# Kernel tuning notes

Hardware: AMD Instinct MI355X
Metric: run time of the kernel (lower is better)

The kernel has to match this reference:

```python
import jax, jax.numpy as jnp
import numpy as np

N = 100000       # nodes
E = 1600000      # edges (avg degree 16)
IN_DIM = 128
HIDDEN = 128


def _glorot(key, shape):
    s = 1.0 / np.sqrt(shape[0])
    return jax.random.uniform(key, shape, minval=-s, maxval=s, dtype=jnp.float32)


def setup_inputs() -> dict:
    key = jax.random.key(0)
    ks = jax.random.split(key, 8)
    x = jax.random.normal(ks[0], (N, IN_DIM), dtype=jnp.float32)
    edge_index = jax.random.randint(ks[1], (2, E), 0, N, dtype=jnp.int32)
    W0 = _glorot(ks[2], (IN_DIM, HIDDEN))
    b0 = jnp.zeros((HIDDEN,), dtype=jnp.float32)
    W1 = _glorot(ks[3], (HIDDEN, HIDDEN))
    b1 = jnp.zeros((HIDDEN,), dtype=jnp.float32)
    W2 = _glorot(ks[4], (HIDDEN, HIDDEN))
    b2 = jnp.zeros((HIDDEN,), dtype=jnp.float32)
    return {"x": x, "edge_index": edge_index,
            "W0": W0, "b0": b0, "W1": W1, "b1": b1, "W2": W2, "b2": b2}


def _gcn_conv(x, row, col, norm, W, b):
    # x' = W x, then out[i] = sum_{j in N(i) U {i}} norm_ji * x'[j], + bias
    h = x @ W                              # [N, out]
    msg = norm[:, None] * h[row]           # [E+N, out] gather + scale
    out = jax.ops.segment_sum(msg, col, num_segments=N)  # scatter-add
    return out + b


def reference(x, edge_index, W0, b0, W1, b1, W2, b2):
    # PyG GCNConv default: add self-loops, symmetric normalization D^-1/2 A D^-1/2
    self_loops = jnp.arange(N, dtype=edge_index.dtype)
    row = jnp.concatenate([edge_index[0], self_loops])  # sources
    col = jnp.concatenate([edge_index[1], self_loops])  # destinations
    deg = jax.ops.segment_sum(jnp.ones_like(col, dtype=x.dtype), col, num_segments=N)
    dinv = jax.lax.rsqrt(deg)              # deg >= 1 thanks to self-loops
    norm = dinv[row] * dinv[col]           # [E+N]

    h = _gcn_conv(x, row, col, norm, W0, b0)
    h = jax.nn.relu(h)                     # dropout: eval mode (identity)
    h = _gcn_conv(h, row, col, norm, W1, b1)
    h = jax.nn.relu(h)
    return _gcn_conv(h, row, col, norm, W2, b2)
```

## Files before the change

### kernel.cpp

```cpp
#include <hip/hip_runtime.h>

#define HID 128
#define BR  128
#define FILL_CHUNK 2048

typedef _Float16 f16;
typedef f16 f16x2 __attribute__((ext_vector_type(2)));
typedef f16 f16x4 __attribute__((ext_vector_type(4)));
typedef f16 f16x8 __attribute__((ext_vector_type(8)));
typedef float f32x4 __attribute__((ext_vector_type(4)));

static __device__ __forceinline__ float2 h2f(unsigned int u) {
    f16x2 v;
    __builtin_memcpy(&v, &u, 4);
    return make_float2((float)v[0], (float)v[1]);
}


__global__ void k_deg_count(const int* __restrict__ col, int* __restrict__ cnt, int E) {
    int e = blockIdx.x * 256 + threadIdx.x;
    if (e < E) atomicAdd(&cnt[col[e]], 1);
}

__global__ void k_scan_block(const int* __restrict__ cnt, int* __restrict__ excl,
                             int* __restrict__ bsum, float* __restrict__ dinv, int N) {
    __shared__ int s[256];
    int i = blockIdx.x * 256 + threadIdx.x;
    int v = (i < N) ? cnt[i] : 0;
    if (i < N) dinv[i] = 1.0f / sqrtf((float)(v + 1));
    s[threadIdx.x] = v;
    __syncthreads();
    for (int off = 1; off < 256; off <<= 1) {
        int t = (threadIdx.x >= off) ? s[threadIdx.x - off] : 0;
        __syncthreads();
        s[threadIdx.x] += t;
        __syncthreads();
    }
    if (i < N) excl[i] = s[threadIdx.x] - v;
    if (threadIdx.x == 255) bsum[blockIdx.x] = s[255];
}

__global__ __launch_bounds__(1024) void k_scan_bsum(int* __restrict__ bsum, int nb) {
    __shared__ int s[1024];
    int i = threadIdx.x;
    int v = (i < nb) ? bsum[i] : 0;
    s[i] = v;
    __syncthreads();
    for (int off = 1; off < 1024; off <<= 1) {
        int t = (i >= off) ? s[i - off] : 0;
        __syncthreads();
        s[i] += t;
        __syncthreads();
    }
    if (i < nb) bsum[i] = s[i] - v;
}

__global__ void k_scan_add(int* __restrict__ row_ptr, const int* __restrict__ bsum,
                           int* __restrict__ fill, int N, int E) {
    int i = blockIdx.x * 256 + threadIdx.x;
    if (i < N) {
        int v = row_ptr[i] + bsum[blockIdx.x];
        row_ptr[i] = v;
        fill[i] = v;
    }
    if (i == 0) row_ptr[N] = E;
}

__global__ void k_fill(const int* __restrict__ row, const int* __restrict__ col,
                       int* __restrict__ fill, int* __restrict__ csr_src, int E, int N) {
    const int xcd = blockIdx.x & 7;
    const int chunk = blockIdx.x >> 3;
    const int per = (N + 7) >> 3;
    const int lo = xcd * per;
    const int hi = min(N, lo + per);
    const int eend = min(E, (chunk + 1) * FILL_CHUNK);
    for (int e = chunk * FILL_CHUNK + threadIdx.x; e < eend; e += 256) {
        int c = col[e];
        if (c >= lo && c < hi) {
            int p = atomicAdd(&fill[c], 1);
            csr_src[p] = row[e];
        }
    }
}


__global__ void k_wprep(const float* __restrict__ W, f16* __restrict__ out) {
    int i = blockIdx.x * 256 + threadIdx.x;
    if (i >= 4096) return;
    int k = i >> 5, n0 = (i & 31) * 4;
    float4 v = reinterpret_cast<const float4*>(W)[i];
    float vv[4] = {v.x, v.y, v.z, v.w};
#pragma unroll
    for (int e = 0; e < 4; ++e) {
        int n = n0 + e;
        int idx = (k >> 3) * 1024 + n * 8 + (k & 7);
        f16 h = (f16)vv[e];
        out[idx] = h;
        out[16384 + idx] = (f16)(vv[e] - (float)h);
    }
}


template<int MODE>
__global__ __launch_bounds__(512, 4) void k_gemm(const void* __restrict__ Xv,
                                                 const f16* __restrict__ Wt,
                                                 const float* __restrict__ dinv,
                                                 f16* __restrict__ H, int N) {
    __shared__ f16 Xs[MODE == 0 ? 2 * 16384 : 16384];
    const int t = threadIdx.x;
    const int row0 = blockIdx.x * BR;

    const int w  = t >> 6;
    const int l  = t & 63;
    const int lg = l >> 4;
    const int li = l & 15;
    const int rg = w >> 2;
    const int cg = w & 3;

    f16x8 Bh[2][4], Bl[2][4];
#pragma unroll
    for (int cb = 0; cb < 2; ++cb) {
        const int ncol = cg * 32 + cb * 16 + li;
#pragma unroll
        for (int ks = 0; ks < 4; ++ks) {
            const int idx = (ks * 4 + lg) * 1024 + ncol * 8;
            Bh[cb][ks] = *reinterpret_cast<const f16x8*>(&Wt[idx]);
            Bl[cb][ks] = *reinterpret_cast<const f16x8*>(&Wt[16384 + idx]);
        }
    }

    if constexpr (MODE == 0) {
        const float* X = (const float*)Xv;
        for (int i = t; i < 4096; i += 512) {
            int r = i >> 5, q = i & 31;
            int gr = row0 + r;
            float4 v = make_float4(0.f, 0.f, 0.f, 0.f);
            if (gr < N) v = reinterpret_cast<const float4*>(X + (size_t)gr * HID)[q];
            f16 h0 = (f16)v.x, h1 = (f16)v.y, h2 = (f16)v.z, h3 = (f16)v.w;
            f16 l0 = (f16)(v.x - (float)h0), l1 = (f16)(v.y - (float)h1);
            f16 l2 = (f16)(v.z - (float)h2), l3 = (f16)(v.w - (float)h3);
            int base = r * 128 + (((q >> 1) ^ (r & 7)) * 8) + (q & 1) * 4;
            *reinterpret_cast<f16x4*>(&Xs[base])         = (f16x4){h0, h1, h2, h3};
            *reinterpret_cast<f16x4*>(&Xs[16384 + base]) = (f16x4){l0, l1, l2, l3};
        }
    } else {
        const f16* X = (const f16*)Xv;
        for (int i = t; i < 2048; i += 512) {
            int r = i >> 4, q = i & 15;
            int gr = row0 + r;
            f16x8 v = {};
            if (gr < N) v = *reinterpret_cast<const f16x8*>(X + (size_t)gr * HID + q * 8);
#pragma unroll
            for (int e = 0; e < 8; ++e) v[e] = v[e] > (f16)0 ? v[e] : (f16)0;
            *reinterpret_cast<f16x8*>(&Xs[r * 128 + ((q ^ (r & 7)) * 8)]) = v;
        }
    }
    __syncthreads();

    f32x4 acc[4][2];
#pragma unroll
    for (int rb = 0; rb < 4; ++rb)
#pragma unroll
        for (int cb = 0; cb < 2; ++cb) acc[rb][cb] = (f32x4){0.f, 0.f, 0.f, 0.f};

#pragma unroll
    for (int rb = 0; rb < 4; ++rb) {
        const int arow = rg * 64 + rb * 16 + li;
#pragma unroll
        for (int ks = 0; ks < 4; ++ks) {
            const int idx = arow * 128 + (((ks * 4 + lg) ^ (arow & 7)) * 8);
            f16x8 Ah = *reinterpret_cast<const f16x8*>(&Xs[idx]);
#pragma unroll
            for (int cb = 0; cb < 2; ++cb) {
                acc[rb][cb] = __builtin_amdgcn_mfma_f32_16x16x32_f16(Ah, Bh[cb][ks], acc[rb][cb], 0, 0, 0);
                acc[rb][cb] = __builtin_amdgcn_mfma_f32_16x16x32_f16(Ah, Bl[cb][ks], acc[rb][cb], 0, 0, 0);
            }
            if constexpr (MODE == 0) {
                f16x8 Al = *reinterpret_cast<const f16x8*>(&Xs[16384 + idx]);
#pragma unroll
                for (int cb = 0; cb < 2; ++cb)
                    acc[rb][cb] = __builtin_amdgcn_mfma_f32_16x16x32_f16(Al, Bh[cb][ks], acc[rb][cb], 0, 0, 0);
            }
        }
    }

#pragma unroll
    for (int rb = 0; rb < 4; ++rb) {
#pragma unroll
        for (int r = 0; r < 4; ++r) {
            const int grow = row0 + rg * 64 + rb * 16 + lg * 4 + r;
            if (grow < N) {
                const float d = dinv[grow];
#pragma unroll
                for (int cb = 0; cb < 2; ++cb)
                    H[(size_t)grow * HID + cg * 32 + cb * 16 + li] = (f16)(acc[rb][cb][r] * d);
            }
        }
    }
}


template<bool F16OUT>
__global__ __launch_bounds__(256) void k_agg_csr(const f16* __restrict__ h,
                                                 const int* __restrict__ csr_src,
                                                 const int* __restrict__ row_ptr,
                                                 const float* __restrict__ dinv,
                                                 const float* __restrict__ bias,
                                                 void* __restrict__ outv, int N) {
    int node = (blockIdx.x * 256 + threadIdx.x) >> 6;
    if (node >= N) return;
    int lane = threadIdx.x & 63;
    const unsigned int* h32 = reinterpret_cast<const unsigned int*>(h);

    float2 self = h2f(h32[(size_t)node * 64 + lane]);
    float accx = self.x, accy = self.y;

    int j = row_ptr[node];
    const int end = row_ptr[node + 1];

    for (; j + 8 <= end; j += 8) {
        int s0 = csr_src[j];
        int s1 = csr_src[j + 1];
        int s2 = csr_src[j + 2];
        int s3 = csr_src[j + 3];
        int s4 = csr_src[j + 4];
        int s5 = csr_src[j + 5];
        int s6 = csr_src[j + 6];
        int s7 = csr_src[j + 7];
        unsigned int u0 = h32[(size_t)s0 * 64 + lane];
        unsigned int u1 = h32[(size_t)s1 * 64 + lane];
        unsigned int u2 = h32[(size_t)s2 * 64 + lane];
        unsigned int u3 = h32[(size_t)s3 * 64 + lane];
        unsigned int u4 = h32[(size_t)s4 * 64 + lane];
        unsigned int u5 = h32[(size_t)s5 * 64 + lane];
        unsigned int u6 = h32[(size_t)s6 * 64 + lane];
        unsigned int u7 = h32[(size_t)s7 * 64 + lane];
        float2 v0 = h2f(u0), v1 = h2f(u1), v2 = h2f(u2), v3 = h2f(u3);
        float2 v4 = h2f(u4), v5 = h2f(u5), v6 = h2f(u6), v7 = h2f(u7);
        accx += ((v0.x + v1.x) + (v2.x + v3.x)) + ((v4.x + v5.x) + (v6.x + v7.x));
        accy += ((v0.y + v1.y) + (v2.y + v3.y)) + ((v4.y + v5.y) + (v6.y + v7.y));
    }
    for (; j < end; ++j) {
        float2 v = h2f(h32[(size_t)csr_src[j] * 64 + lane]);
        accx += v.x;
        accy += v.y;
    }

    float di = dinv[node];
    int c = lane * 2;
    float ox = fmaf(di, accx, bias[c]);
    float oy = fmaf(di, accy, bias[c + 1]);
    if constexpr (F16OUT) {
        f16x2 o = {(f16)ox, (f16)oy};
        *reinterpret_cast<f16x2*>((f16*)outv + (size_t)node * HID + c) = o;
    } else {
        *reinterpret_cast<float2*>((float*)outv + (size_t)node * HID + c) = make_float2(ox, oy);
    }
}


extern "C" void kernel_launch(void* const* d_in, const int* in_sizes, int n_in,
                              void* d_out, int out_size, void* d_ws, size_t ws_size,
                              hipStream_t stream) {
    const float* x  = (const float*)d_in[0];
    const int*   ei = (const int*)  d_in[1];
    const float* W0 = (const float*)d_in[2];
    const float* b0 = (const float*)d_in[3];
    const float* W1 = (const float*)d_in[4];
    const float* b1 = (const float*)d_in[5];
    const float* W2 = (const float*)d_in[6];
    const float* b2 = (const float*)d_in[7];

    const int N = in_sizes[0] / HID;
    const int E = in_sizes[1] / 2;
    const int* row = ei;
    const int* col = ei + E;

    const int nb_n = (N + 255) / 256;

    f16*   h16     = (f16*)d_ws;
    float* dinv    = (float*)(h16 + (size_t)N * HID);
    int*   cnt     = (int*)(dinv + N);
    int*   row_ptr = cnt + N;
    int*   fill    = row_ptr + (N + 1);
    int*   bsum    = fill + N;
    int*   csr_src = bsum + nb_n;
    f16*   wt0     = (f16*)(csr_src + E);
    f16*   wt1     = wt0 + 32768;
    f16*   wt2     = wt1 + 32768;
    f16*   act     = (f16*)d_out;
    float* out     = (float*)d_out;

    const int nb_e    = (E + 255) / 256;
    const int nb_gemm = (N + BR - 1) / BR;
    const int nb_agg  = (N * 64 + 255) / 256;
    const int nb_fill = ((E + FILL_CHUNK - 1) / FILL_CHUNK) * 8;

    hipMemsetAsync(cnt, 0, (size_t)N * sizeof(int), stream);
    k_wprep<<<16, 256, 0, stream>>>(W0, wt0);
    k_wprep<<<16, 256, 0, stream>>>(W1, wt1);
    k_wprep<<<16, 256, 0, stream>>>(W2, wt2);
    k_deg_count <<<nb_e, 256, 0, stream>>>(col, cnt, E);
    k_scan_block<<<nb_n, 256, 0, stream>>>(cnt, row_ptr, bsum, dinv, N);
    k_scan_bsum <<<1, 1024, 0, stream>>>(bsum, nb_n);
    k_scan_add  <<<nb_n, 256, 0, stream>>>(row_ptr, bsum, fill, N, E);
    k_fill      <<<nb_fill, 256, 0, stream>>>(row, col, fill, csr_src, E, N);

    k_gemm<0>      <<<nb_gemm, 512, 0, stream>>>(x, wt0, dinv, h16, N);
    k_agg_csr<true><<<nb_agg, 256, 0, stream>>>(h16, csr_src, row_ptr, dinv, b0, act, N);
    k_gemm<1>      <<<nb_gemm, 512, 0, stream>>>(act, wt1, dinv, h16, N);
    k_agg_csr<true><<<nb_agg, 256, 0, stream>>>(h16, csr_src, row_ptr, dinv, b1, act, N);
    k_gemm<1>      <<<nb_gemm, 512, 0, stream>>>(act, wt2, dinv, h16, N);
    k_agg_csr<false><<<nb_agg, 256, 0, stream>>>(h16, csr_src, row_ptr, dinv, b2, out, N);
}
```

Measured before the change: 455.5 us.

## Partition degree-count atomics by XCD, merge weight prep, transpose GEMM output

The degree-count kernel now uses the same XCD-partitioned chunking as the fill kernel, so each block only issues atomics for destination nodes in its XCD's range, keeping those atomics local to one L2. The three weight-prep launches are merged into a single launch. The GEMM swaps its MFMA operand order (W as A, X as B), so each lane holds four consecutive output columns of one row and can write them as one 8-byte f16x4 store instead of scattered 2-byte stores. The cost is that every block now reads all of `col`, eight times the column-index traffic in the degree-count pass.

Result: no change. 450.7 us (-1.1%).

```diff
diff --git a/kernel.cpp b/kernel.cpp
--- a/kernel.cpp
+++ b/kernel.cpp
@@ -17,9 +17,17 @@
 }
 
 
-__global__ void k_deg_count(const int* __restrict__ col, int* __restrict__ cnt, int E) {
-    int e = blockIdx.x * 256 + threadIdx.x;
-    if (e < E) atomicAdd(&cnt[col[e]], 1);
+__global__ void k_deg_count(const int* __restrict__ col, int* __restrict__ cnt, int E, int N) {
+    const int xcd = blockIdx.x & 7;
+    const int chunk = blockIdx.x >> 3;
+    const int per = (N + 7) >> 3;
+    const int lo = xcd * per;
+    const int hi = min(N, lo + per);
+    const int eend = min(E, (chunk + 1) * FILL_CHUNK);
+    for (int e = chunk * FILL_CHUNK + threadIdx.x; e < eend; e += 256) {
+        int c = col[e];
+        if (c >= lo && c < hi) atomicAdd(&cnt[c], 1);
+    }
 }
 
 __global__ void k_scan_block(const int* __restrict__ cnt, int* __restrict__ excl,
@@ -84,9 +92,13 @@
 }
 
 
-__global__ void k_wprep(const float* __restrict__ W, f16* __restrict__ out) {
-    int i = blockIdx.x * 256 + threadIdx.x;
-    if (i >= 4096) return;
+__global__ void k_wprep3(const float* __restrict__ W0, const float* __restrict__ W1,
+                         const float* __restrict__ W2, f16* __restrict__ out) {
+    const int b = blockIdx.x;
+    const int which = b >> 4;
+    const float* W = which == 0 ? W0 : (which == 1 ? W1 : W2);
+    f16* o = out + which * 32768;
+    int i = (b & 15) * 256 + threadIdx.x;
     int k = i >> 5, n0 = (i & 31) * 4;
     float4 v = reinterpret_cast<const float4*>(W)[i];
     float vv[4] = {v.x, v.y, v.z, v.w};
@@ -95,8 +107,8 @@
         int n = n0 + e;
         int idx = (k >> 3) * 1024 + n * 8 + (k & 7);
         f16 h = (f16)vv[e];
-        out[idx] = h;
-        out[16384 + idx] = (f16)(vv[e] - (float)h);
+        o[idx] = h;
+        o[16384 + idx] = (f16)(vv[e] - (float)h);
     }
 }
 
@@ -114,18 +126,18 @@
     const int l  = t & 63;
     const int lg = l >> 4;
     const int li = l & 15;
-    const int rg = w >> 2;
-    const int cg = w & 3;
-
-    f16x8 Bh[2][4], Bl[2][4];
-#pragma unroll
-    for (int cb = 0; cb < 2; ++cb) {
-        const int ncol = cg * 32 + cb * 16 + li;
+    const int ng = w & 3;
+    const int mg = w >> 2;
+
+    f16x8 Wh[2][4], Wl[2][4];
+#pragma unroll
+    for (int nb = 0; nb < 2; ++nb) {
+        const int ncol = (ng * 2 + nb) * 16 + li;
 #pragma unroll
         for (int ks = 0; ks < 4; ++ks) {
             const int idx = (ks * 4 + lg) * 1024 + ncol * 8;
-            Bh[cb][ks] = *reinterpret_cast<const f16x8*>(&Wt[idx]);
-            Bl[cb][ks] = *reinterpret_cast<const f16x8*>(&Wt[16384 + idx]);
+            Wh[nb][ks] = *reinterpret_cast<const f16x8*>(&Wt[idx]);
+            Wl[nb][ks] = *reinterpret_cast<const f16x8*>(&Wt[16384 + idx]);
         }
     }
 
@@ -157,43 +169,43 @@
     }
     __syncthreads();
 
-    f32x4 acc[4][2];
-#pragma unroll
-    for (int rb = 0; rb < 4; ++rb)
-#pragma unroll
-        for (int cb = 0; cb < 2; ++cb) acc[rb][cb] = (f32x4){0.f, 0.f, 0.f, 0.f};
-
-#pragma unroll
-    for (int rb = 0; rb < 4; ++rb) {
-        const int arow = rg * 64 + rb * 16 + li;
+    f32x4 acc[2][4];
+#pragma unroll
+    for (int nb = 0; nb < 2; ++nb)
+#pragma unroll
+        for (int mb = 0; mb < 4; ++mb) acc[nb][mb] = (f32x4){0.f, 0.f, 0.f, 0.f};
+
+#pragma unroll
+    for (int mb = 0; mb < 4; ++mb) {
+        const int arow = mg * 64 + mb * 16 + li;
 #pragma unroll
         for (int ks = 0; ks < 4; ++ks) {
             const int idx = arow * 128 + (((ks * 4 + lg) ^ (arow & 7)) * 8);
-            f16x8 Ah = *reinterpret_cast<const f16x8*>(&Xs[idx]);
-#pragma unroll
-            for (int cb = 0; cb < 2; ++cb) {
-                acc[rb][cb] = __builtin_amdgcn_mfma_f32_16x16x32_f16(Ah, Bh[cb][ks], acc[rb][cb], 0, 0, 0);
-                acc[rb][cb] = __builtin_amdgcn_mfma_f32_16x16x32_f16(Ah, Bl[cb][ks], acc[rb][cb], 0, 0, 0);
+            f16x8 Xh = *reinterpret_cast<const f16x8*>(&Xs[idx]);
+#pragma unroll
+            for (int nb = 0; nb < 2; ++nb) {
+                acc[nb][mb] = __builtin_amdgcn_mfma_f32_16x16x32_f16(Wh[nb][ks], Xh, acc[nb][mb], 0, 0, 0);
+                acc[nb][mb] = __builtin_amdgcn_mfma_f32_16x16x32_f16(Wl[nb][ks], Xh, acc[nb][mb], 0, 0, 0);
             }
             if constexpr (MODE == 0) {
-                f16x8 Al = *reinterpret_cast<const f16x8*>(&Xs[16384 + idx]);
-#pragma unroll
-                for (int cb = 0; cb < 2; ++cb)
-                    acc[rb][cb] = __builtin_amdgcn_mfma_f32_16x16x32_f16(Al, Bh[cb][ks], acc[rb][cb], 0, 0, 0);
+                f16x8 Xl = *reinterpret_cast<const f16x8*>(&Xs[16384 + idx]);
+#pragma unroll
+                for (int nb = 0; nb < 2; ++nb)
+                    acc[nb][mb] = __builtin_amdgcn_mfma_f32_16x16x32_f16(Wh[nb][ks], Xl, acc[nb][mb], 0, 0, 0);
             }
         }
     }
 
 #pragma unroll
-    for (int rb = 0; rb < 4; ++rb) {
-#pragma unroll
-        for (int r = 0; r < 4; ++r) {
-            const int grow = row0 + rg * 64 + rb * 16 + lg * 4 + r;
-            if (grow < N) {
-                const float d = dinv[grow];
-#pragma unroll
-                for (int cb = 0; cb < 2; ++cb)
-                    H[(size_t)grow * HID + cg * 32 + cb * 16 + li] = (f16)(acc[rb][cb][r] * d);
+    for (int mb = 0; mb < 4; ++mb) {
+        const int m = row0 + mg * 64 + mb * 16 + li;
+        if (m < N) {
+            const float d = dinv[m];
+#pragma unroll
+            for (int nb = 0; nb < 2; ++nb) {
+                f16x4 o = {(f16)(acc[nb][mb][0] * d), (f16)(acc[nb][mb][1] * d),
+                           (f16)(acc[nb][mb][2] * d), (f16)(acc[nb][mb][3] * d)};
+                *reinterpret_cast<f16x4*>(&H[(size_t)m * HID + (ng * 2 + nb) * 16 + lg * 4]) = o;
             }
         }
     }
@@ -285,22 +297,20 @@
     int*   fill    = row_ptr + (N + 1);
     int*   bsum    = fill + N;
     int*   csr_src = bsum + nb_n;
-    f16*   wt0     = (f16*)(csr_src + E);
-    f16*   wt1     = wt0 + 32768;
-    f16*   wt2     = wt1 + 32768;
+    f16*   wt      = (f16*)(csr_src + E);
+    f16*   wt0     = wt;
+    f16*   wt1     = wt + 32768;
+    f16*   wt2     = wt + 65536;
     f16*   act     = (f16*)d_out;
     float* out     = (float*)d_out;
 
-    const int nb_e    = (E + 255) / 256;
     const int nb_gemm = (N + BR - 1) / BR;
     const int nb_agg  = (N * 64 + 255) / 256;
     const int nb_fill = ((E + FILL_CHUNK - 1) / FILL_CHUNK) * 8;
 
     hipMemsetAsync(cnt, 0, (size_t)N * sizeof(int), stream);
-    k_wprep<<<16, 256, 0, stream>>>(W0, wt0);
-    k_wprep<<<16, 256, 0, stream>>>(W1, wt1);
-    k_wprep<<<16, 256, 0, stream>>>(W2, wt2);
-    k_deg_count <<<nb_e, 256, 0, stream>>>(col, cnt, E);
+    k_wprep3<<<48, 256, 0, stream>>>(W0, W1, W2, wt);
+    k_deg_count <<<nb_fill, 256, 0, stream>>>(col, cnt, E, N);
     k_scan_block<<<nb_n, 256, 0, stream>>>(cnt, row_ptr, bsum, dinv, N);
     k_scan_bsum <<<1, 1024, 0, stream>>>(bsum, nb_n);
     k_scan_add  <<<nb_n, 256, 0, stream>>>(row_ptr, bsum, fill, N, E);
```
